# Kernel tuning notes

Measured on AMD Instinct MI355X. Metric: run time of the kernel, lower is better.

Reference implementation:

```python
import jax, jax.numpy as jnp
import numpy as np
import math

NEG_BIG = -1e9

def setup_inputs() -> dict:
    key = jax.random.key(0)
    k1, k2, k3 = jax.random.split(key, 3)
    N, C, T = 16, 64, 2048
    qkv = jax.random.normal(k1, (N, 3 * C, T), dtype=jnp.float32)
    pos = jax.random.normal(k2, (N, C, T), dtype=jnp.float32)
    attn_mask = jax.random.randint(k3, (N, T, T), 0, 2) == 1  # bool mask, True = masked
    return {"qkv": qkv, "pos": pos, "attn_mask": attn_mask}

def reference(qkv, pos, attn_mask):
    ch = qkv.shape[1] // 3
    q, k, v = jnp.split(qkv, 3, axis=1)  # each [N, C, T]
    q = q + pos
    k = k + pos
    v = v + pos
    scale = 1.0 / math.sqrt(math.sqrt(ch))
    # [N, T, T] attention logits
    weight = jnp.einsum('bct,bcs->bts', q * scale, k * scale)
    weight = jnp.where(attn_mask, NEG_BIG, weight)
    weight = jax.nn.softmax(weight.astype(jnp.float32), axis=-1).astype(weight.dtype)
    return jnp.einsum('bts,bcs->bct', weight, v)
```

## Files before the change

### kernel.cpp

```cpp
#include <hip/hip_runtime.h>
#include <hip/hip_bf16.h>

typedef float f32x4 __attribute__((ext_vector_type(4)));
typedef unsigned int u32x4 __attribute__((ext_vector_type(4)));
typedef short s16x8 __attribute__((ext_vector_type(8)));

#define L2E 1.44269504088896340736f

static __device__ __forceinline__ unsigned int bf16_rne(float f) {
    unsigned int u = __builtin_bit_cast(unsigned int, f);
    return (u + 0x7fffu + ((u >> 16) & 1u)) >> 16;
}
static __device__ __forceinline__ unsigned int pack_bf16x2(float lo, float hi) {
    return bf16_rne(lo) | (bf16_rne(hi) << 16);
}
static __device__ __forceinline__ unsigned int cvt_pk_bf16(float lo, float hi) {
    unsigned int r;
    asm("v_cvt_pk_bf16_f32 %0, %1, %2" : "=v"(r) : "v"(lo), "v"(hi));
    return r;
}

__global__ __launch_bounds__(256) void qkv_prep(const float* __restrict__ qkv,
                                                const float* __restrict__ pos,
                                                unsigned short* __restrict__ qs,
                                                unsigned short* __restrict__ ktf,
                                                unsigned short* __restrict__ vtf)
{
    __shared__ unsigned short QtS[64][72];
    __shared__ unsigned short KtS[64][72];
    const int b    = blockIdx.y;
    const int t0   = blockIdx.x * 64;
    const int i    = threadIdx.x;
    const int crow = i >> 2;
    const int t16  = (i & 3) * 16;
    const float QSCALE = 0.125f * L2E;

    float pr[16];
    {
        const f32x4* pp = reinterpret_cast<const f32x4*>(
            pos + ((size_t)(b * 64 + crow)) * 2048 + t0 + t16);
        #pragma unroll
        for (int j = 0; j < 4; ++j) {
            f32x4 v = __builtin_nontemporal_load(pp + j);
            pr[4*j+0] = v[0]; pr[4*j+1] = v[1]; pr[4*j+2] = v[2]; pr[4*j+3] = v[3];
        }
    }
    const float* qp = qkv + ((size_t)(b * 192 + crow)) * 2048 + t0 + t16;
    {
        #pragma unroll
        for (int j = 0; j < 4; ++j) {
            f32x4 v = __builtin_nontemporal_load(reinterpret_cast<const f32x4*>(qp) + j);
            #pragma unroll
            for (int e = 0; e < 4; ++e)
                QtS[t16 + 4*j + e][crow] =
                    (unsigned short)bf16_rne((v[e] + pr[4*j+e]) * QSCALE);
        }
    }
    {
        const float* kp = qp + (size_t)64 * 2048;
        #pragma unroll
        for (int j = 0; j < 4; ++j) {
            f32x4 v = __builtin_nontemporal_load(reinterpret_cast<const f32x4*>(kp) + j);
            #pragma unroll
            for (int e = 0; e < 4; ++e)
                KtS[t16 + 4*j + e][crow] =
                    (unsigned short)bf16_rne(v[e] + pr[4*j+e]);
        }
    }
    {
        const float* vp = qp + (size_t)128 * 2048;
        unsigned int vv[8];
        #pragma unroll
        for (int j = 0; j < 4; ++j) {
            f32x4 v = __builtin_nontemporal_load(reinterpret_cast<const f32x4*>(vp) + j);
            vv[2*j+0] = pack_bf16x2(v[0] + pr[4*j+0], v[1] + pr[4*j+1]);
            vv[2*j+1] = pack_bf16x2(v[2] + pr[4*j+2], v[3] + pr[4*j+3]);
        }
        const int n   = crow >> 4;
        const int lnv = crow & 15;
        const int sb  = t0 >> 6;
        #pragma unroll
        for (int h = 0; h < 2; ++h) {
            const int soff = t16 + 8 * h;
            const int kc2  = soff >> 5;
            const int lgv  = (soff >> 3) & 3;
            unsigned short* dst = vtf +
                ((((size_t)(b * 32 + sb)) * 4 + n) * 2 + kc2) * 512 +
                (lnv + 16 * lgv) * 8;
            *reinterpret_cast<u32x4*>(dst) =
                (u32x4){vv[4*h+0], vv[4*h+1], vv[4*h+2], vv[4*h+3]};
        }
    }
    __syncthreads();
    {
        const int trow = i >> 2;
        const int c16  = (i & 3) * 16;
        u32x4 a0 = *reinterpret_cast<const u32x4*>(&QtS[trow][c16]);
        u32x4 a1 = *reinterpret_cast<const u32x4*>(&QtS[trow][c16 + 8]);
        unsigned short* qd = qs + ((size_t)(b * 2048 + t0 + trow)) * 64 + c16;
        reinterpret_cast<u32x4*>(qd)[0] = a0;
        reinterpret_cast<u32x4*>(qd)[1] = a1;
    }
    {
        const int g   = i >> 6;
        const int l   = i & 63;
        const int lnk = l & 15;
        const int lgk = l >> 4;
        #pragma unroll
        for (int kc = 0; kc < 2; ++kc) {
            u32x4 d = *reinterpret_cast<const u32x4*>(
                &KtS[16 * g + lnk][32 * kc + 8 * lgk]);
            unsigned short* dst = ktf +
                (((size_t)(b * 128 + (t0 >> 4) + g)) * 2 + kc) * 512 + l * 8;
            *reinterpret_cast<u32x4*>(dst) = d;
        }
    }
}

__global__ __launch_bounds__(256) void mask_pack(const void* __restrict__ maskp,
                                                 unsigned short* __restrict__ mbits)
{
    const int b   = blockIdx.y;
    const int row = blockIdx.x * 2 + (threadIdx.x >> 7);
    const int c16 = threadIdx.x & 127;

    unsigned int accm = 0;
    {
        const unsigned int* mu = (const unsigned int*)maskp;
        #pragma unroll
        for (int j = 0; j < 16; ++j) accm |= mu[j];
    }
    unsigned int v = 0;
    const size_t rowbase = (size_t)b * 2048 + (size_t)row;
    if ((accm & 0xffffff00u) != 0u) {
        u32x4 x = *reinterpret_cast<const u32x4*>(
            (const unsigned char*)maskp + rowbase * 2048 + c16 * 16);
        #pragma unroll
        for (int w = 0; w < 4; ++w)
            #pragma unroll
            for (int e = 0; e < 4; ++e)
                v |= (((x[w] >> (8 * e)) & 0xffu) ? 1u : 0u) << (4 * w + e);
    } else {
        const u32x4* src = reinterpret_cast<const u32x4*>(
            (const unsigned int*)maskp + rowbase * 2048 + c16 * 16);
        #pragma unroll
        for (int w = 0; w < 4; ++w) {
            u32x4 x = src[w];
            #pragma unroll
            for (int e = 0; e < 4; ++e)
                v |= (x[e] ? 1u : 0u) << (4 * w + e);
        }
    }
    mbits[rowbase * 128 + c16] = (unsigned short)v;
}

__global__ __launch_bounds__(256) void attn_kernel(const unsigned short* __restrict__ qs,
                                                   const unsigned short* __restrict__ ktf,
                                                   const unsigned short* __restrict__ vtf,
                                                   const unsigned short* __restrict__ mbits,
                                                   float* __restrict__ out)
{
    __shared__ unsigned short KldsF[2][4096];
    __shared__ unsigned short VldsF[2][4096];

    const int b    = blockIdx.y;
    const int t0   = blockIdx.x * 64;
    const int tid  = threadIdx.x;
    const int wave = tid >> 6;
    const int lane = tid & 63;
    const int ln   = lane & 15;
    const int lg   = lane >> 4;
    const int tg   = t0 + 16 * wave + ln;

    s16x8 qf[2];
    #pragma unroll
    for (int kc = 0; kc < 2; ++kc)
        qf[kc] = *reinterpret_cast<const s16x8*>(
            qs + ((size_t)(b * 2048 + tg)) * 64 + 32 * kc + 8 * lg);

    f32x4 acc[4];
    #pragma unroll
    for (int n = 0; n < 4; ++n) acc[n] = (f32x4){0.f, 0.f, 0.f, 0.f};
    float L = 0.0f;

    const unsigned short* kbase = ktf + ((size_t)b * 256) * 512;
    const unsigned short* vbase = vtf + ((size_t)b * 32) * 4096;
    const unsigned short* mrowp = mbits + ((size_t)b * 2048 + (size_t)tg) * 128;

    unsigned long long mq_cur;

    {
        u32x4 k0 = *reinterpret_cast<const u32x4*>(kbase + tid * 8);
        u32x4 k1 = *reinterpret_cast<const u32x4*>(kbase + 2048 + tid * 8);
        u32x4 v0 = *reinterpret_cast<const u32x4*>(vbase + tid * 8);
        u32x4 v1 = *reinterpret_cast<const u32x4*>(vbase + 2048 + tid * 8);
        mq_cur = *reinterpret_cast<const unsigned long long*>(mrowp);
        *reinterpret_cast<u32x4*>(&KldsF[0][tid * 8])        = k0;
        *reinterpret_cast<u32x4*>(&KldsF[0][2048 + tid * 8]) = k1;
        *reinterpret_cast<u32x4*>(&VldsF[0][tid * 8])        = v0;
        *reinterpret_cast<u32x4*>(&VldsF[0][2048 + tid * 8]) = v1;
    }
    __syncthreads();

    int cur = 0;
    for (int st = 0; st < 32; ++st) {
        u32x4 k0, k1, v0, v1;
        unsigned long long mq_nxt;
        const bool pf = (st < 31);
        if (pf) {
            const unsigned short* ks = kbase + (size_t)(st + 1) * 4096;
            const unsigned short* vs = vbase + (size_t)(st + 1) * 4096;
            k0 = *reinterpret_cast<const u32x4*>(ks + tid * 8);
            k1 = *reinterpret_cast<const u32x4*>(ks + 2048 + tid * 8);
            v0 = *reinterpret_cast<const u32x4*>(vs + tid * 8);
            v1 = *reinterpret_cast<const u32x4*>(vs + 2048 + tid * 8);
            mq_nxt = *reinterpret_cast<const unsigned long long*>(mrowp + (st + 1) * 4);
        }

        f32x4 S[4];
        #pragma unroll
        for (int ti = 0; ti < 4; ++ti) S[ti] = (f32x4){0.f, 0.f, 0.f, 0.f};
        __builtin_amdgcn_s_setprio(1);
        #pragma unroll
        for (int kc = 0; kc < 2; ++kc) {
            #pragma unroll
            for (int ti = 0; ti < 4; ++ti) {
                s16x8 kf = *reinterpret_cast<const s16x8*>(
                    &KldsF[cur][(ti * 2 + kc) * 512 + lane * 8]);
                S[ti] = __builtin_amdgcn_mfma_f32_16x16x32_bf16(kf, qf[kc], S[ti], 0, 0, 0);
            }
        }
        __builtin_amdgcn_s_setprio(0);

        const unsigned long long shq = mq_cur >> (4 * lg);
        const unsigned int wlo = (unsigned int)shq;
        const unsigned int whi = (unsigned int)(shq >> 32);
        float p[4][4];
        #pragma unroll
        for (int ti = 0; ti < 4; ++ti) {
            const unsigned int w = (ti < 2) ? wlo : whi;
            const int base = 16 * (ti & 1);
            #pragma unroll
            for (int r = 0; r < 4; ++r) {
                const float s = ((w >> (base + r)) & 1u) ? -16384.0f : S[ti][r];
                p[ti][r] = __builtin_amdgcn_exp2f(s);
                L += p[ti][r];
            }
        }

        unsigned int pk[4][2];
        #pragma unroll
        for (int ti = 0; ti < 4; ++ti) {
            pk[ti][0] = cvt_pk_bf16(p[ti][0], p[ti][1]);
            pk[ti][1] = cvt_pk_bf16(p[ti][2], p[ti][3]);
        }
        unsigned int pfr[2][4];
        #pragma unroll
        for (int kc2 = 0; kc2 < 2; ++kc2) {
            #pragma unroll
            for (int b2 = 0; b2 < 2; ++b2) {
                unsigned int x = pk[2 * kc2 + 0][b2];
                unsigned int y = pk[2 * kc2 + 1][b2];
                asm("v_permlane32_swap_b32 %0, %1" : "+v"(x), "+v"(y));
                asm("v_permlane16_swap_b32 %0, %1" : "+v"(x), "+v"(y));
                pfr[kc2][0 + b2] = x;
                pfr[kc2][2 + b2] = y;
            }
        }

        __builtin_amdgcn_s_setprio(1);
        #pragma unroll
        for (int kc2 = 0; kc2 < 2; ++kc2) {
            union { unsigned int u[4]; s16x8 s; } pu;
            pu.u[0] = pfr[kc2][0]; pu.u[1] = pfr[kc2][1];
            pu.u[2] = pfr[kc2][2]; pu.u[3] = pfr[kc2][3];
            #pragma unroll
            for (int n = 0; n < 4; ++n) {
                s16x8 vf = *reinterpret_cast<const s16x8*>(
                    &VldsF[cur][(n * 2 + kc2) * 512 + lane * 8]);
                acc[n] = __builtin_amdgcn_mfma_f32_16x16x32_bf16(vf, pu.s, acc[n], 0, 0, 0);
            }
        }
        __builtin_amdgcn_s_setprio(0);

        if (pf) {
            *reinterpret_cast<u32x4*>(&KldsF[cur ^ 1][tid * 8])        = k0;
            *reinterpret_cast<u32x4*>(&KldsF[cur ^ 1][2048 + tid * 8]) = k1;
            *reinterpret_cast<u32x4*>(&VldsF[cur ^ 1][tid * 8])        = v0;
            *reinterpret_cast<u32x4*>(&VldsF[cur ^ 1][2048 + tid * 8]) = v1;
            mq_cur = mq_nxt;
            __syncthreads();
            cur ^= 1;
        }
    }

    float Lr = L;
    Lr += __shfl_xor(Lr, 16, 64);
    Lr += __shfl_xor(Lr, 32, 64);
    const float inv = 1.0f / Lr;
    #pragma unroll
    for (int n = 0; n < 4; ++n)
        #pragma unroll
        for (int r = 0; r < 4; ++r)
            __builtin_nontemporal_store(
                acc[n][r] * inv,
                &out[((size_t)(b * 64 + 16 * n + 4 * lg + r)) * 2048 + tg]);
}

extern "C" void kernel_launch(void* const* d_in, const int* in_sizes, int n_in,
                              void* d_out, int out_size, void* d_ws, size_t ws_size,
                              hipStream_t stream) {
    const float* qkv = (const float*)d_in[0];
    const float* pos = (const float*)d_in[1];
    const void*  msk = d_in[2];
    float* outp = (float*)d_out;
    unsigned short* ws = (unsigned short*)d_ws;
    const size_t PLANE = (size_t)16 * 2048 * 64;
    unsigned short* qs    = ws;
    unsigned short* ktf   = ws + PLANE;
    unsigned short* vtf   = ws + 2 * PLANE;
    unsigned short* mbits = ws + 3 * PLANE;

    dim3 grid(2048 / 64, 16);
    qkv_prep <<<grid, 256, 0, stream>>>(qkv, pos, qs, ktf, vtf);
    mask_pack<<<dim3(1024, 16), 256, 0, stream>>>(msk, mbits);
    attn_kernel<<<grid, 256, 0, stream>>>(qs, ktf, vtf, mbits, outp);
}
```

Before: 94.94 us.

## Split attention over two key chunks and combine partial sums in a separate kernel

The attention kernel gains a third grid dimension that divides the 2048 keys into two halves. Each block streams 16 K/V tiles instead of 32 and writes its unnormalized accumulator and row sum to workspace. A new combine kernel adds the two partials and divides by the summed normalizers. This doubles the number of blocks to fill the GPU better, at the cost of roughly 16 MB of extra partial writes and reads plus one more kernel launch.

```diff
diff --git a/kernel.cpp b/kernel.cpp
--- a/kernel.cpp
+++ b/kernel.cpp
@@ -158,19 +158,21 @@
                                                    const unsigned short* __restrict__ ktf,
                                                    const unsigned short* __restrict__ vtf,
                                                    const unsigned short* __restrict__ mbits,
-                                                   float* __restrict__ out)
+                                                   float* __restrict__ accw,
+                                                   float* __restrict__ Lw)
 {
     __shared__ unsigned short KldsF[2][4096];
     __shared__ unsigned short VldsF[2][4096];
 
-    const int b    = blockIdx.y;
-    const int t0   = blockIdx.x * 64;
-    const int tid  = threadIdx.x;
-    const int wave = tid >> 6;
-    const int lane = tid & 63;
-    const int ln   = lane & 15;
-    const int lg   = lane >> 4;
-    const int tg   = t0 + 16 * wave + ln;
+    const int b     = blockIdx.y;
+    const int t0    = blockIdx.x * 64;
+    const int chunk = blockIdx.z;
+    const int tid   = threadIdx.x;
+    const int wave  = tid >> 6;
+    const int lane  = tid & 63;
+    const int ln    = lane & 15;
+    const int lg    = lane >> 4;
+    const int tg    = t0 + 16 * wave + ln;
 
     s16x8 qf[2];
     #pragma unroll
@@ -183,9 +185,12 @@
     for (int n = 0; n < 4; ++n) acc[n] = (f32x4){0.f, 0.f, 0.f, 0.f};
     float L = 0.0f;
 
-    const unsigned short* kbase = ktf + ((size_t)b * 256) * 512;
-    const unsigned short* vbase = vtf + ((size_t)b * 32) * 4096;
-    const unsigned short* mrowp = mbits + ((size_t)b * 2048 + (size_t)tg) * 128;
+    const unsigned short* kbase = ktf + ((size_t)b * 256) * 512
+                                      + (size_t)chunk * 16 * 4096;
+    const unsigned short* vbase = vtf + ((size_t)b * 32) * 4096
+                                      + (size_t)chunk * 16 * 4096;
+    const unsigned short* mrowp = mbits + ((size_t)b * 2048 + (size_t)tg) * 128
+                                        + chunk * 64;
 
     unsigned long long mq_cur;
 
@@ -203,10 +208,10 @@
     __syncthreads();
 
     int cur = 0;
-    for (int st = 0; st < 32; ++st) {
+    for (int st = 0; st < 16; ++st) {
         u32x4 k0, k1, v0, v1;
         unsigned long long mq_nxt;
-        const bool pf = (st < 31);
+        const bool pf = (st < 15);
         if (pf) {
             const unsigned short* ks = kbase + (size_t)(st + 1) * 4096;
             const unsigned short* vs = vbase + (size_t)(st + 1) * 4096;
@@ -297,14 +302,44 @@
     float Lr = L;
     Lr += __shfl_xor(Lr, 16, 64);
     Lr += __shfl_xor(Lr, 32, 64);
-    const float inv = 1.0f / Lr;
+    Lw[((size_t)(chunk * 16 + b)) * 2048 + tg] = Lr;
     #pragma unroll
     for (int n = 0; n < 4; ++n)
         #pragma unroll
         for (int r = 0; r < 4; ++r)
             __builtin_nontemporal_store(
-                acc[n][r] * inv,
-                &out[((size_t)(b * 64 + 16 * n + 4 * lg + r)) * 2048 + tg]);
+                acc[n][r],
+                &accw[((size_t)((chunk * 16 + b) * 64 + 16 * n + 4 * lg + r)) * 2048 + tg]);
+}
+
+__global__ __launch_bounds__(256) void combine_kernel(const float* __restrict__ accw,
+                                                      const float* __restrict__ Lw,
+                                                      float* __restrict__ out)
+{
+    const int c = blockIdx.x;
+    const int b = blockIdx.y;
+    const int t = threadIdx.x * 8;
+
+    const size_t r0 = ((size_t)(b * 64 + c)) * 2048 + t;
+    const size_t r1 = ((size_t)((16 + b) * 64 + c)) * 2048 + t;
+    const size_t l0 = ((size_t)b) * 2048 + t;
+    const size_t l1 = ((size_t)(16 + b)) * 2048 + t;
+
+    #pragma unroll
+    for (int h = 0; h < 2; ++h) {
+        f32x4 a0 = *reinterpret_cast<const f32x4*>(accw + r0 + 4 * h);
+        f32x4 a1 = *reinterpret_cast<const f32x4*>(accw + r1 + 4 * h);
+        f32x4 s0 = *reinterpret_cast<const f32x4*>(Lw + l0 + 4 * h);
+        f32x4 s1 = *reinterpret_cast<const f32x4*>(Lw + l1 + 4 * h);
+        f32x4 o;
+        #pragma unroll
+        for (int e = 0; e < 4; ++e)
+            o[e] = (a0[e] + a1[e]) / (s0[e] + s1[e]);
+        __builtin_nontemporal_store(o[0], out + r0 + 4 * h + 0);
+        __builtin_nontemporal_store(o[1], out + r0 + 4 * h + 1);
+        __builtin_nontemporal_store(o[2], out + r0 + 4 * h + 2);
+        __builtin_nontemporal_store(o[3], out + r0 + 4 * h + 3);
+    }
 }
 
 extern "C" void kernel_launch(void* const* d_in, const int* in_sizes, int n_in,
@@ -320,9 +355,12 @@
     unsigned short* ktf   = ws + PLANE;
     unsigned short* vtf   = ws + 2 * PLANE;
     unsigned short* mbits = ws + 3 * PLANE;
+    float* accw = (float*)(ws + 3 * PLANE + (size_t)16 * 2048 * 128);
+    float* Lw   = accw + (size_t)2 * 16 * 64 * 2048;
 
     dim3 grid(2048 / 64, 16);
     qkv_prep <<<grid, 256, 0, stream>>>(qkv, pos, qs, ktf, vtf);
     mask_pack<<<dim3(1024, 16), 256, 0, stream>>>(msk, mbits);
-    attn_kernel<<<grid, 256, 0, stream>>>(qs, ktf, vtf, mbits, outp);
-}
+    attn_kernel<<<dim3(32, 16, 2), 256, 0, stream>>>(qs, ktf, vtf, mbits, accw, Lw);
+    combine_kernel<<<dim3(64, 16), 256, 0, stream>>>(accw, Lw, outp);
+}
```

Result: slower. 102.3 us (+7.8%).
